# Performance work log

Measured on AMD Instinct MI355X. Metric: run time of the kernel, lower is better.

Reference implementation:

```python
import jax, jax.numpy as jnp
import numpy as np

H = 2048
EPS = 1e-5  # torch LayerNorm default

def layer_norm(x, g, b):
    mu = jnp.mean(x, axis=-1, keepdims=True)
    var = jnp.mean(jnp.square(x - mu), axis=-1, keepdims=True)
    return (x - mu) * jax.lax.rsqrt(var + EPS) * g + b

def setup_inputs() -> dict:
    key = jax.random.key(0)
    ks = jax.random.split(key, 5)
    bound = 1.0 / np.sqrt(H)  # torch Linear default init range
    x = jax.random.normal(ks[0], (8192, H), dtype=jnp.float32)
    W1 = jax.random.uniform(ks[1], (H, H), jnp.float32, -bound, bound)
    b1 = jax.random.uniform(ks[2], (H,), jnp.float32, -bound, bound)
    W2 = jax.random.uniform(ks[3], (H, H), jnp.float32, -bound, bound)
    b2 = jax.random.uniform(ks[4], (H,), jnp.float32, -bound, bound)
    g1 = jnp.ones((H,), jnp.float32); be1 = jnp.zeros((H,), jnp.float32)
    g2 = jnp.ones((H,), jnp.float32); be2 = jnp.zeros((H,), jnp.float32)
    return {"x": x, "W1": W1, "b1": b1, "W2": W2, "b2": b2,
            "g1": g1, "be1": be1, "g2": g2, "be2": be2}

def reference(x, W1, b1, W2, b2, g1, be1, g2, be2):
    # ln1 -> linear1 -> relu -> (dropout p=0) -> ln2 -> linear2 -> (dropout p=0) -> +x -> relu
    out = layer_norm(x, g1, be1)
    out = jax.nn.relu(out @ W1.T + b1)
    out = layer_norm(out, g2, be2)
    out = out @ W2.T + b2
    return jax.nn.relu(out + x)
```

## Files before the change

### kernel.cpp

```cpp
#include <hip/hip_runtime.h>
#include <hip/hip_bf16.h>

#define H_DIM 2048
#define LN_EPS 1e-5f

typedef __bf16 bf16_t;
typedef __bf16 bf16x4 __attribute__((ext_vector_type(4)));
typedef __bf16 bf16x8 __attribute__((ext_vector_type(8)));
typedef float f32x4 __attribute__((ext_vector_type(4)));

__device__ __forceinline__ void async_copy16(const void* g, void* l) {
    __builtin_amdgcn_global_load_lds((const __attribute__((address_space(1))) void*)g,
                                     (__attribute__((address_space(3))) void*)l,
                                     16, 0, 0);
}

#define FENCE() asm volatile("" ::: "memory")
#define BARRIER() do { FENCE(); __builtin_amdgcn_s_barrier(); FENCE(); } while (0)

__global__ __launch_bounds__(256) void pre_kernel(const float* __restrict__ w1,
                                                  const float* __restrict__ w2,
                                                  bf16_t* __restrict__ o1,
                                                  bf16_t* __restrict__ o2,
                                                  const float* __restrict__ x,
                                                  const float* __restrict__ g,
                                                  const float* __restrict__ b,
                                                  bf16_t* __restrict__ lnb,
                                                  bf16_t* __restrict__ xb) {
    const int bid = blockIdx.x, t = threadIdx.x;
    if (bid < 8192) {
        const int n4 = (H_DIM * H_DIM) / 4;
        int i = bid * 256 + t;
        const float* src; bf16_t* dst; int j;
        if (i < n4) { src = w1; dst = o1; j = i; }
        else        { src = w2; dst = o2; j = i - n4; }
        float4 v = reinterpret_cast<const float4*>(src)[j];
        bf16x4 r;
        r[0] = (bf16_t)v.x; r[1] = (bf16_t)v.y; r[2] = (bf16_t)v.z; r[3] = (bf16_t)v.w;
        reinterpret_cast<bf16x4*>(dst)[j] = r;
        return;
    }
    const int l = t & 63, w = t >> 6;
    const size_t row = (size_t)(bid - 8192) * 4 + w;
    const float* xr = x + row * H_DIM;
    float4 v[8];
    #pragma unroll
    for (int k = 0; k < 8; ++k) v[k] = reinterpret_cast<const float4*>(xr)[l + k * 64];
    float s = 0.f, s2 = 0.f;
    #pragma unroll
    for (int k = 0; k < 8; ++k) {
        s  += v[k].x + v[k].y + v[k].z + v[k].w;
        s2 += v[k].x * v[k].x + v[k].y * v[k].y + v[k].z * v[k].z + v[k].w * v[k].w;
    }
    #pragma unroll
    for (int off = 32; off > 0; off >>= 1) {
        s  += __shfl_down(s,  off, 64);
        s2 += __shfl_down(s2, off, 64);
    }
    s  = __shfl(s,  0, 64);
    s2 = __shfl(s2, 0, 64);
    float mu   = s * (1.f / H_DIM);
    float rstd = rsqrtf(s2 * (1.f / H_DIM) - mu * mu + LN_EPS);
    bf16_t* orow = lnb + row * H_DIM;
    bf16_t* xrow = xb ? xb + row * H_DIM : nullptr;
    #pragma unroll
    for (int k = 0; k < 8; ++k) {
        int c = l + k * 64;
        float4 gv = reinterpret_cast<const float4*>(g)[c];
        float4 bv = reinterpret_cast<const float4*>(b)[c];
        bf16x4 y;
        y[0] = (bf16_t)((v[k].x - mu) * rstd * gv.x + bv.x);
        y[1] = (bf16_t)((v[k].y - mu) * rstd * gv.y + bv.y);
        y[2] = (bf16_t)((v[k].z - mu) * rstd * gv.z + bv.z);
        y[3] = (bf16_t)((v[k].w - mu) * rstd * gv.w + bv.w);
        reinterpret_cast<bf16x4*>(orow)[c] = y;
        if (xrow) {
            bf16x4 xv;
            xv[0] = (bf16_t)v[k].x; xv[1] = (bf16_t)v[k].y;
            xv[2] = (bf16_t)v[k].z; xv[3] = (bf16_t)v[k].w;
            reinterpret_cast<bf16x4*>(xrow)[c] = xv;
        }
    }
}

__global__ __launch_bounds__(256) void ln_bf16_v2(const bf16_t* __restrict__ in,
                                                  const float* __restrict__ g,
                                                  const float* __restrict__ b,
                                                  bf16_t* __restrict__ out) {
    const int l = threadIdx.x & 63, w = threadIdx.x >> 6;
    const size_t row = (size_t)blockIdx.x * 4 + w;
    const bf16_t* xr = in + row * H_DIM;
    bf16x8 xv[4];
    #pragma unroll
    for (int k = 0; k < 4; ++k) xv[k] = reinterpret_cast<const bf16x8*>(xr)[l + k * 64];
    float vv[32];
    #pragma unroll
    for (int k = 0; k < 4; ++k)
        #pragma unroll
        for (int j = 0; j < 8; ++j) vv[k * 8 + j] = (float)xv[k][j];
    float s = 0.f, s2 = 0.f;
    #pragma unroll
    for (int e = 0; e < 32; ++e) { s += vv[e]; s2 += vv[e] * vv[e]; }
    #pragma unroll
    for (int off = 32; off > 0; off >>= 1) {
        s  += __shfl_down(s,  off, 64);
        s2 += __shfl_down(s2, off, 64);
    }
    s  = __shfl(s,  0, 64);
    s2 = __shfl(s2, 0, 64);
    float mu   = s * (1.f / H_DIM);
    float rstd = rsqrtf(s2 * (1.f / H_DIM) - mu * mu + LN_EPS);
    bf16_t* orow = out + row * H_DIM;
    #pragma unroll
    for (int k = 0; k < 4; ++k) {
        int c = l + k * 64;
        float4 g0 = reinterpret_cast<const float4*>(g)[c * 2];
        float4 g1 = reinterpret_cast<const float4*>(g)[c * 2 + 1];
        float4 b0 = reinterpret_cast<const float4*>(b)[c * 2];
        float4 b1 = reinterpret_cast<const float4*>(b)[c * 2 + 1];
        bf16x8 y;
        y[0] = (bf16_t)((vv[k*8+0] - mu) * rstd * g0.x + b0.x);
        y[1] = (bf16_t)((vv[k*8+1] - mu) * rstd * g0.y + b0.y);
        y[2] = (bf16_t)((vv[k*8+2] - mu) * rstd * g0.z + b0.z);
        y[3] = (bf16_t)((vv[k*8+3] - mu) * rstd * g0.w + b0.w);
        y[4] = (bf16_t)((vv[k*8+4] - mu) * rstd * g1.x + b1.x);
        y[5] = (bf16_t)((vv[k*8+5] - mu) * rstd * g1.y + b1.y);
        y[6] = (bf16_t)((vv[k*8+6] - mu) * rstd * g1.z + b1.z);
        y[7] = (bf16_t)((vv[k*8+7] - mu) * rstd * g1.w + b1.w);
        reinterpret_cast<bf16x8*>(orow)[c] = y;
    }
}

#define LDW 88
#define RPW 264

template<int FINAL, int RB>
__global__ __launch_bounds__(512, 2) void gemm8_kernel(
    const bf16_t* __restrict__ A,
    const bf16_t* __restrict__ B,
    const float*  __restrict__ bias,
    const float*  __restrict__ residf,
    const bf16_t* __restrict__ residb,
    bf16_t* __restrict__ obf,
    float*  __restrict__ of)
{
    __shared__ bf16_t sm[8 * 8192];

    const int tid = threadIdx.x;
    const int l  = tid & 63, w = tid >> 6;
    const int wm = w >> 2,  wn = w & 3;
    const int cl = l & 15,  ch = l >> 4;

    const int cpx = gridDim.x >> 3;
    const int bid = blockIdx.x;
    const int swz = (bid & 7) * cpx + (bid >> 3);
    const size_t row0 = (size_t)(swz >> 3) * 256;
    const size_t col0 = (size_t)(swz & 7) * 256;

    const bf16_t* Abase = A + row0 * H_DIM;
    const bf16_t* Bbase = B + col0 * H_DIM;

    const int rr  = w * 8 + (l >> 3);
    const int scb = (l & 7) ^ (l >> 3);
    const size_t soff  = (size_t)rr * H_DIM + scb * 8;
    const int ldsw0 = w * 512;
    const int ldsw1 = 4096 + w * 512;

    const int swx = cl & 7;
    const int cbks[2] = { ch ^ swx, (4 + ch) ^ swx };

    float bv[4];
    #pragma unroll
    for (int n = 0; n < 4; ++n) bv[n] = bias[col0 + wn * 64 + n * 16 + cl];

    f32x4 acc[2][4][4] = {};

    auto STAGE = [&](const bf16_t* Gb, int kt, int half, int region) {
        const bf16_t* g = Gb + (size_t)half * (128 * H_DIM) + kt * 64 + soff;
        bf16_t* s = &sm[region * 8192];
        async_copy16(g,               s + ldsw0);
        async_copy16(g + 64 * H_DIM,  s + ldsw1);
    };
    auto RDA = [&](int buf, int mh, int m, int ks) -> bf16x8 {
        int r = mh * 64 + m * 16 + cl;
        return *(const bf16x8*)&sm[(buf * 4 + wm) * 8192 + r * 64 + cbks[ks] * 8];
    };
    auto RDB = [&](int buf, int n, int ks) -> bf16x8 {
        int r = (wn & 1) * 64 + n * 16 + cl;
        return *(const bf16x8*)&sm[(buf * 4 + 2 + (wn >> 1)) * 8192 + r * 64 + cbks[ks] * 8];
    };

    auto KT = [&](int buf, int t, bool stA, bool stB, int vm) {
        bf16x8 a0[4], a1[4], b0[4], b1[4];
        #pragma unroll
        for (int n = 0; n < 4; ++n) { b0[n] = RDB(buf, n, 0); b1[n] = RDB(buf, n, 1); }
        #pragma unroll
        for (int m = 0; m < 4; ++m) { a0[m] = RDA(buf, 0, m, 0); a1[m] = RDA(buf, 0, m, 1); }
        if (stA) { STAGE(Abase, t + 1, 0, (buf ^ 1) * 4 + 0);
                   STAGE(Abase, t + 1, 1, (buf ^ 1) * 4 + 1); }
        BARRIER();
        __builtin_amdgcn_s_setprio(1);
        #pragma unroll
        for (int m = 0; m < 4; ++m)
            #pragma unroll
            for (int n = 0; n < 4; ++n)
                acc[0][m][n] = __builtin_amdgcn_mfma_f32_16x16x32_bf16(a0[m], b0[n], acc[0][m][n], 0, 0, 0);
        #pragma unroll
        for (int m = 0; m < 4; ++m)
            #pragma unroll
            for (int n = 0; n < 4; ++n)
                acc[0][m][n] = __builtin_amdgcn_mfma_f32_16x16x32_bf16(a1[m], b1[n], acc[0][m][n], 0, 0, 0);
        __builtin_amdgcn_s_setprio(0);
        BARRIER();
        #pragma unroll
        for (int m = 0; m < 4; ++m) { a0[m] = RDA(buf, 1, m, 0); a1[m] = RDA(buf, 1, m, 1); }
        if (stB) { STAGE(Bbase, t + 2, 0, buf * 4 + 2);
                   STAGE(Bbase, t + 2, 1, buf * 4 + 3); }
        BARRIER();
        __builtin_amdgcn_s_setprio(1);
        #pragma unroll
        for (int m = 0; m < 4; ++m)
            #pragma unroll
            for (int n = 0; n < 4; ++n)
                acc[1][m][n] = __builtin_amdgcn_mfma_f32_16x16x32_bf16(a0[m], b0[n], acc[1][m][n], 0, 0, 0);
        #pragma unroll
        for (int m = 0; m < 4; ++m)
            #pragma unroll
            for (int n = 0; n < 4; ++n)
                acc[1][m][n] = __builtin_amdgcn_mfma_f32_16x16x32_bf16(a1[m], b1[n], acc[1][m][n], 0, 0, 0);
        __builtin_amdgcn_s_setprio(0);
        if (vm == 4)      asm volatile("s_waitcnt vmcnt(4)");
        else if (vm == 0) asm volatile("s_waitcnt vmcnt(0)");
        BARRIER();
    };

    STAGE(Abase, 0, 0, 0); STAGE(Abase, 0, 1, 1);
    STAGE(Bbase, 0, 0, 2); STAGE(Bbase, 0, 1, 3);
    STAGE(Bbase, 1, 0, 6); STAGE(Bbase, 1, 1, 7);
    asm volatile("s_waitcnt vmcnt(4)");
    BARRIER();

    for (int t = 0; t < 30; t += 2) {
        KT(0, t,     true, true, 4);
        KT(1, t + 1, true, true, 4);
    }
    KT(0, 30, true,  false, 0);
    KT(1, 31, false, false, -1);

    if constexpr (FINAL) {
        if constexpr (RB) {
            #pragma unroll
            for (int p = 0; p < 2; ++p) {
                #pragma unroll
                for (int i = 0; i < 8; ++i) {
                    int c = i * 512 + tid;
                    int u = c >> 5, cb = c & 31;
                    size_t gr = row0 + (size_t)(u >> 6) * 128 + p * 64 + (u & 63);
                    bf16x8 vv = *(const bf16x8*)&residb[gr * H_DIM + col0 + cb * 8];
                    *(bf16x8*)&sm[u * RPW + cb * 8] = vv;
                }
                BARRIER();
                #pragma unroll
                for (int m = 0; m < 4; ++m)
                    #pragma unroll
                    for (int n = 0; n < 4; ++n) {
                        size_t col = col0 + wn * 64 + n * 16 + cl;
                        #pragma unroll
                        for (int j = 0; j < 4; ++j) {
                            int u = wm * 64 + m * 16 + ch * 4 + j;
                            size_t row = row0 + wm * 128 + p * 64 + m * 16 + ch * 4 + j;
                            float rv = (float)sm[u * RPW + wn * 64 + n * 16 + cl];
                            of[row * H_DIM + col] = fmaxf(acc[p][m][n][j] + bv[n] + rv, 0.f);
                        }
                    }
                BARRIER();
            }
        } else {
            #pragma unroll
            for (int mh = 0; mh < 2; ++mh)
                #pragma unroll
                for (int m = 0; m < 4; ++m)
                    #pragma unroll
                    for (int n = 0; n < 4; ++n) {
                        size_t col = col0 + wn * 64 + n * 16 + cl;
                        #pragma unroll
                        for (int j = 0; j < 4; ++j) {
                            size_t row = row0 + wm * 128 + mh * 64 + m * 16 + ch * 4 + j;
                            size_t idx = row * H_DIM + col;
                            of[idx] = fmaxf(acc[mh][m][n][j] + bv[n] + residf[idx], 0.f);
                        }
                    }
        }
    } else {
        bf16_t* wls = (bf16_t*)((char*)sm + w * (64 * LDW * 2));
        #pragma unroll
        for (int mh = 0; mh < 2; ++mh) {
            #pragma unroll
            for (int m = 0; m < 4; ++m)
                #pragma unroll
                for (int n = 0; n < 4; ++n)
                    #pragma unroll
                    for (int j = 0; j < 4; ++j) {
                        int lr = m * 16 + ch * 4 + j;
                        int lc = n * 16 + cl;
                        wls[lr * LDW + lc] = (bf16_t)fmaxf(acc[mh][m][n][j] + bv[n], 0.f);
                    }
            #pragma unroll
            for (int k = 0; k < 8; ++k) {
                int c = l + k * 64;
                int r = c >> 3, cb = c & 7;
                bf16x8 vv = *(const bf16x8*)&wls[r * LDW + cb * 8];
                size_t grow = row0 + wm * 128 + mh * 64 + r;
                *(bf16x8*)&obf[grow * H_DIM + col0 + wn * 64 + cb * 8] = vv;
            }
        }
    }
}

extern "C" void kernel_launch(void* const* d_in, const int* in_sizes, int n_in,
                              void* d_out, int out_size, void* d_ws, size_t ws_size,
                              hipStream_t stream) {
    const float* x   = (const float*)d_in[0];
    const float* W1  = (const float*)d_in[1];
    const float* b1  = (const float*)d_in[2];
    const float* W2  = (const float*)d_in[3];
    const float* b2  = (const float*)d_in[4];
    const float* g1  = (const float*)d_in[5];
    const float* be1 = (const float*)d_in[6];
    const float* g2  = (const float*)d_in[7];
    const float* be2 = (const float*)d_in[8];
    float* out = (float*)d_out;

    const int M = in_sizes[0] / H_DIM;

    char* ws = (char*)d_ws;
    bf16_t* W1b = (bf16_t*)(ws);
    bf16_t* W2b = (bf16_t*)(ws + (8u << 20));
    bf16_t* lnb = (bf16_t*)(ws + (16u << 20));
    bf16_t* h1  = (bf16_t*)(ws + (48u << 20));
    const bool use_xb = ws_size >= ((size_t)96 << 20);
    bf16_t* xb  = use_xb ? (bf16_t*)(ws + (80u << 20)) : nullptr;

    pre_kernel<<<dim3(8192 + M / 4), dim3(256), 0, stream>>>(
        W1, W2, W1b, W2b, x, g1, be1, lnb, xb);

    gemm8_kernel<0, 0><<<dim3((M / 256) * 8), dim3(512), 0, stream>>>(
        lnb, W1b, b1, nullptr, nullptr, h1, nullptr);

    ln_bf16_v2<<<dim3(M / 4), dim3(256), 0, stream>>>(h1, g2, be2, lnb);

    if (use_xb) {
        gemm8_kernel<1, 1><<<dim3((M / 256) * 8), dim3(512), 0, stream>>>(
            lnb, W2b, b2, nullptr, xb, nullptr, out);
    } else {
        gemm8_kernel<1, 0><<<dim3((M / 256) * 8), dim3(512), 0, stream>>>(
            lnb, W2b, b2, x, nullptr, nullptr, out);
    }
}
```

Before: 297.0 us.

## Split K-tile MFMA phases finer and prefetch residual into registers early

Each K-tile step is split into four phases instead of two. Every phase loads only one k-slice of A/B fragments and issues one async stage copy, which roughly halves the live fragment registers and spreads global-to-LDS copies across more barriers. The residual tile for the fused epilogue is also loaded into registers before the last two K-tiles, so its global latency overlaps with compute. This adds more barriers per tile and 16 extra live bf16x8 registers during the tail, which may raise register pressure or synchronisation cost.

```diff
diff --git a/kernel.cpp b/kernel.cpp
--- a/kernel.cpp
+++ b/kernel.cpp
@@ -191,43 +191,57 @@
     };
 
     auto KT = [&](int buf, int t, bool stA, bool stB, int vm) {
-        bf16x8 a0[4], a1[4], b0[4], b1[4];
-        #pragma unroll
-        for (int n = 0; n < 4; ++n) { b0[n] = RDB(buf, n, 0); b1[n] = RDB(buf, n, 1); }
-        #pragma unroll
-        for (int m = 0; m < 4; ++m) { a0[m] = RDA(buf, 0, m, 0); a1[m] = RDA(buf, 0, m, 1); }
-        if (stA) { STAGE(Abase, t + 1, 0, (buf ^ 1) * 4 + 0);
-                   STAGE(Abase, t + 1, 1, (buf ^ 1) * 4 + 1); }
+        bf16x8 a[4], b0[4], b1[4];
+        #pragma unroll
+        for (int n = 0; n < 4; ++n) b0[n] = RDB(buf, n, 0);
+        #pragma unroll
+        for (int m = 0; m < 4; ++m) a[m] = RDA(buf, 0, m, 0);
+        if (stA) STAGE(Abase, t + 1, 0, (buf ^ 1) * 4 + 0);
         BARRIER();
         __builtin_amdgcn_s_setprio(1);
         #pragma unroll
         for (int m = 0; m < 4; ++m)
             #pragma unroll
             for (int n = 0; n < 4; ++n)
-                acc[0][m][n] = __builtin_amdgcn_mfma_f32_16x16x32_bf16(a0[m], b0[n], acc[0][m][n], 0, 0, 0);
+                acc[0][m][n] = __builtin_amdgcn_mfma_f32_16x16x32_bf16(a[m], b0[n], acc[0][m][n], 0, 0, 0);
+        __builtin_amdgcn_s_setprio(0);
+        BARRIER();
+        #pragma unroll
+        for (int n = 0; n < 4; ++n) b1[n] = RDB(buf, n, 1);
+        #pragma unroll
+        for (int m = 0; m < 4; ++m) a[m] = RDA(buf, 0, m, 1);
+        if (stA) STAGE(Abase, t + 1, 1, (buf ^ 1) * 4 + 1);
+        BARRIER();
+        __builtin_amdgcn_s_setprio(1);
         #pragma unroll
         for (int m = 0; m < 4; ++m)
             #pragma unroll
             for (int n = 0; n < 4; ++n)
-                acc[0][m][n] = __builtin_amdgcn_mfma_f32_16x16x32_bf16(a1[m], b1[n], acc[0][m][n], 0, 0, 0);
+                acc[0][m][n] = __builtin_amdgcn_mfma_f32_16x16x32_bf16(a[m], b1[n], acc[0][m][n], 0, 0, 0);
         __builtin_amdgcn_s_setprio(0);
         BARRIER();
         #pragma unroll
-        for (int m = 0; m < 4; ++m) { a0[m] = RDA(buf, 1, m, 0); a1[m] = RDA(buf, 1, m, 1); }
-        if (stB) { STAGE(Bbase, t + 2, 0, buf * 4 + 2);
-                   STAGE(Bbase, t + 2, 1, buf * 4 + 3); }
+        for (int m = 0; m < 4; ++m) a[m] = RDA(buf, 1, m, 0);
+        if (stB) STAGE(Bbase, t + 2, 0, buf * 4 + 2);
         BARRIER();
         __builtin_amdgcn_s_setprio(1);
         #pragma unroll
         for (int m = 0; m < 4; ++m)
             #pragma unroll
             for (int n = 0; n < 4; ++n)
-                acc[1][m][n] = __builtin_amdgcn_mfma_f32_16x16x32_bf16(a0[m], b0[n], acc[1][m][n], 0, 0, 0);
+                acc[1][m][n] = __builtin_amdgcn_mfma_f32_16x16x32_bf16(a[m], b0[n], acc[1][m][n], 0, 0, 0);
+        __builtin_amdgcn_s_setprio(0);
+        BARRIER();
+        #pragma unroll
+        for (int m = 0; m < 4; ++m) a[m] = RDA(buf, 1, m, 1);
+        if (stB) STAGE(Bbase, t + 2, 1, buf * 4 + 3);
+        BARRIER();
+        __builtin_amdgcn_s_setprio(1);
         #pragma unroll
         for (int m = 0; m < 4; ++m)
             #pragma unroll
             for (int n = 0; n < 4; ++n)
-                acc[1][m][n] = __builtin_amdgcn_mfma_f32_16x16x32_bf16(a1[m], b1[n], acc[1][m][n], 0, 0, 0);
+                acc[1][m][n] = __builtin_amdgcn_mfma_f32_16x16x32_bf16(a[m], b1[n], acc[1][m][n], 0, 0, 0);
         __builtin_amdgcn_s_setprio(0);
         if (vm == 4)      asm volatile("s_waitcnt vmcnt(4)");
         else if (vm == 0) asm volatile("s_waitcnt vmcnt(0)");
@@ -244,6 +258,20 @@
         KT(0, t,     true, true, 4);
         KT(1, t + 1, true, true, 4);
     }
+
+    bf16x8 rrg[16];
+    if constexpr (FINAL && RB) {
+        #pragma unroll
+        for (int p = 0; p < 2; ++p)
+            #pragma unroll
+            for (int i2 = 0; i2 < 8; ++i2) {
+                int c = i2 * 512 + tid;
+                int u = c >> 5, cb = c & 31;
+                size_t gr = row0 + (size_t)(u >> 6) * 128 + p * 64 + (u & 63);
+                rrg[p * 8 + i2] = *(const bf16x8*)&residb[gr * H_DIM + col0 + cb * 8];
+            }
+    }
+
     KT(0, 30, true,  false, 0);
     KT(1, 31, false, false, -1);
 
@@ -252,12 +280,10 @@
             #pragma unroll
             for (int p = 0; p < 2; ++p) {
                 #pragma unroll
-                for (int i = 0; i < 8; ++i) {
-                    int c = i * 512 + tid;
+                for (int i2 = 0; i2 < 8; ++i2) {
+                    int c = i2 * 512 + tid;
                     int u = c >> 5, cb = c & 31;
-                    size_t gr = row0 + (size_t)(u >> 6) * 128 + p * 64 + (u & 63);
-                    bf16x8 vv = *(const bf16x8*)&residb[gr * H_DIM + col0 + cb * 8];
-                    *(bf16x8*)&sm[u * RPW + cb * 8] = vv;
+                    *(bf16x8*)&sm[u * RPW + cb * 8] = rrg[p * 8 + i2];
                 }
                 BARRIER();
                 #pragma unroll
```

New measurement: 301.1 us. No clear change (+1.4%).
